# Kernel optimization log

Hardware: AMD Instinct MI355X
Metric: run time of the kernel (lower is better)

Reference implementation:

```python
import jax, jax.numpy as jnp
import numpy as np

N_HEADS, IN_F, COND_IN, OUT_F = 8, 16, 32, 32
B = 32768


def setup_inputs() -> dict:
    key = jax.random.key(0)
    k1, k2, k3, k4 = jax.random.split(key, 4)
    return {
        "input": jax.random.normal(k1, (N_HEADS, B, IN_F), dtype=jnp.float32),
        "cond": jax.random.normal(k2, (N_HEADS, B, COND_IN), dtype=jnp.float32),
        "cond_weight": jax.random.normal(k3, (N_HEADS, OUT_F * (IN_F + 1), COND_IN), dtype=jnp.float32) * 0.1,
        "cond_bias": jax.random.normal(k4, (N_HEADS, OUT_F * (IN_F + 1)), dtype=jnp.float32) * 0.1,
    }


def reference(input, cond, cond_weight, cond_bias):
    h, b, in_f = input.shape
    out_f = cond_weight.shape[1] // (in_f + 1)
    # hypernetwork: generate per-sample weights (h, b, out*(in+1))
    w = jnp.einsum('hbc,hkc->hbk', cond, cond_weight) + cond_bias[:, None, :]
    w = w.reshape(h, b, out_f, in_f + 1)  # (h, b, out, in+1)
    # append homogeneous 1 for bias column, then per-sample matvec
    x1 = jnp.concatenate([input, jnp.ones((h, b, 1), dtype=input.dtype)], axis=-1)
    return jnp.einsum('hboi,hbi->hbo', w, x1)
```

## Files before the change

kernel.cpp:

```cpp
#include <hip/hip_runtime.h>

#define NH    8
#define BROWS 32768
#define INF   16
#define CIN   32
#define OUTF  32
#define KTOT  544

typedef __attribute__((ext_vector_type(8))) short short8;
typedef __attribute__((ext_vector_type(4))) float floatx4;

__device__ __forceinline__ short f2bf(float f) {
    __bf16 h = (__bf16)f;
    return __builtin_bit_cast(short, h);
}

__global__ __launch_bounds__(256) void meta_multilinear(
    const float* __restrict__ input,
    const float* __restrict__ cond,
    const float* __restrict__ weight,
    const float* __restrict__ bias,
    float* __restrict__ out)
{
    const int tid   = threadIdx.x;
    const int lane  = tid & 63;
    const int wave  = tid >> 6;
    const int pair  = wave >> 1;
    const int otile = wave & 1;
    const int r     = lane & 15;
    const int quad  = lane >> 4;
    const int c0    = quad * 8;

    const int h = blockIdx.y;
    const int o = otile * 16 + r;

    const float* Wh = weight + (size_t)h * KTOT * CIN;
    const float* bh = bias   + (size_t)h * KTOT;

    short8 bfrag[17];
    #pragma unroll
    for (int i = 0; i < 17; ++i) {
        const float* src = Wh + (o * 17 + i) * CIN + c0;
        floatx4 w0 = *(const floatx4*)(src);
        floatx4 w1 = *(const floatx4*)(src + 4);
        short8 f;
        f[0]=f2bf(w0.x); f[1]=f2bf(w0.y); f[2]=f2bf(w0.z); f[3]=f2bf(w0.w);
        f[4]=f2bf(w1.x); f[5]=f2bf(w1.y); f[6]=f2bf(w1.z); f[7]=f2bf(w1.w);
        bfrag[i] = f;
    }

    short8 bbias;
    #pragma unroll
    for (int j = 0; j < 8; ++j) {
        const int i = c0 + j;
        short v = 0;
        if (i < 17) v = f2bf(bh[o * 17 + i]);
        bbias[j] = v;
    }

    const int pairId = blockIdx.x * 2 + pair;

    for (int it = 0; it < 8; ++it) {
        const int b0 = (pairId * 8 + it) * 16;

        const float* crow = cond + ((size_t)h * BROWS + b0 + r) * CIN + c0;
        floatx4 cA = *(const floatx4*)(crow);
        floatx4 cB = *(const floatx4*)(crow + 4);

        const float* xrow = input + ((size_t)h * BROWS + b0 + r) * INF;
        floatx4 x0 = *(const floatx4*)(xrow);
        floatx4 x1v = *(const floatx4*)(xrow + 4);
        floatx4 x2 = *(const floatx4*)(xrow + 8);
        floatx4 x3 = *(const floatx4*)(xrow + 12);
        const float xr[17] = {x0.x,x0.y,x0.z,x0.w, x1v.x,x1v.y,x1v.z,x1v.w,
                              x2.x,x2.y,x2.z,x2.w, x3.x,x3.y,x3.z,x3.w, 1.0f};

        floatx4 acc = {0.f, 0.f, 0.f, 0.f};

        {
            short8 af;
            if (quad == 0) {
                af[0]=f2bf(xr[0]); af[1]=f2bf(xr[1]); af[2]=f2bf(xr[2]); af[3]=f2bf(xr[3]);
                af[4]=f2bf(xr[4]); af[5]=f2bf(xr[5]); af[6]=f2bf(xr[6]); af[7]=f2bf(xr[7]);
            } else if (quad == 1) {
                af[0]=f2bf(xr[8]);  af[1]=f2bf(xr[9]);  af[2]=f2bf(xr[10]); af[3]=f2bf(xr[11]);
                af[4]=f2bf(xr[12]); af[5]=f2bf(xr[13]); af[6]=f2bf(xr[14]); af[7]=f2bf(xr[15]);
            } else if (quad == 2) {
                af[0]=f2bf(1.0f); af[1]=0; af[2]=0; af[3]=0;
                af[4]=0; af[5]=0; af[6]=0; af[7]=0;
            } else {
                af[0]=0; af[1]=0; af[2]=0; af[3]=0;
                af[4]=0; af[5]=0; af[6]=0; af[7]=0;
            }
            acc = __builtin_amdgcn_mfma_f32_16x16x32_bf16(af, bbias, acc, 0, 0, 0);
        }

        #pragma unroll
        for (int i = 0; i < 17; ++i) {
            const float s = xr[i];
            short8 af;
            af[0]=f2bf(cA.x*s); af[1]=f2bf(cA.y*s); af[2]=f2bf(cA.z*s); af[3]=f2bf(cA.w*s);
            af[4]=f2bf(cB.x*s); af[5]=f2bf(cB.y*s); af[6]=f2bf(cB.z*s); af[7]=f2bf(cB.w*s);
            acc = __builtin_amdgcn_mfma_f32_16x16x32_bf16(af, bfrag[i], acc, 0, 0, 0);
        }

        float* orow = out + ((size_t)h * BROWS + b0) * OUTF;
        #pragma unroll
        for (int j = 0; j < 4; ++j) {
            orow[(quad * 4 + j) * OUTF + o] = acc[j];
        }
    }
}

extern "C" void kernel_launch(void* const* d_in, const int* in_sizes, int n_in,
                              void* d_out, int out_size, void* d_ws, size_t ws_size,
                              hipStream_t stream) {
    const float* input  = (const float*)d_in[0];
    const float* cond   = (const float*)d_in[1];
    const float* weight = (const float*)d_in[2];
    const float* bias   = (const float*)d_in[3];
    float* out = (float*)d_out;

    dim3 grid(128, NH, 1);
    dim3 block(256, 1, 1);
    hipLaunchKernelGGL(meta_multilinear, grid, block, 0, stream,
                       input, cond, weight, bias, out);
}
```

Before: 133.7 us.

## Swap MFMA operands so output is transposed and scale per-column results by x

Restructures the per-sample computation so cond is converted to bf16 once per tile instead of being scaled by each input element before conversion. Each weight column's MFMA output is scaled by the input scalar in fp32 and accumulated into two alternating accumulators. The swapped operand order makes each lane own contiguous output columns, which allows vectorized 16-byte stores. The grid is doubled with half the iterations per wave, and launch bounds request higher occupancy. This adds fp32 vector FMAs after each MFMA in exchange for removing the per-element multiply and convert work.

```diff
diff --git a/kernel.cpp b/kernel.cpp
--- a/kernel.cpp
+++ b/kernel.cpp
@@ -15,7 +15,7 @@
     return __builtin_bit_cast(short, h);
 }
 
-__global__ __launch_bounds__(256) void meta_multilinear(
+__global__ __launch_bounds__(256, 3) void meta_multilinear(
     const float* __restrict__ input,
     const float* __restrict__ cond,
     const float* __restrict__ weight,
@@ -37,7 +37,7 @@
     const float* Wh = weight + (size_t)h * KTOT * CIN;
     const float* bh = bias   + (size_t)h * KTOT;
 
-    short8 bfrag[17];
+    short8 wfrag[17];
     #pragma unroll
     for (int i = 0; i < 17; ++i) {
         const float* src = Wh + (o * 17 + i) * CIN + c0;
@@ -46,69 +46,77 @@
         short8 f;
         f[0]=f2bf(w0.x); f[1]=f2bf(w0.y); f[2]=f2bf(w0.z); f[3]=f2bf(w0.w);
         f[4]=f2bf(w1.x); f[5]=f2bf(w1.y); f[6]=f2bf(w1.z); f[7]=f2bf(w1.w);
-        bfrag[i] = f;
+        wfrag[i] = f;
     }
 
-    short8 bbias;
+    short8 bA;
     #pragma unroll
     for (int j = 0; j < 8; ++j) {
         const int i = c0 + j;
         short v = 0;
         if (i < 17) v = f2bf(bh[o * 17 + i]);
-        bbias[j] = v;
+        bA[j] = v;
     }
 
     const int pairId = blockIdx.x * 2 + pair;
+    const int bbase  = pairId * 64;
 
-    for (int it = 0; it < 8; ++it) {
-        const int b0 = (pairId * 8 + it) * 16;
+    const float* condh = cond  + (size_t)h * BROWS * CIN;
+    const float* inh   = input + (size_t)h * BROWS * INF;
+    const floatx4 zero = {0.f, 0.f, 0.f, 0.f};
 
-        const float* crow = cond + ((size_t)h * BROWS + b0 + r) * CIN + c0;
+    #pragma unroll
+    for (int it = 0; it < 4; ++it) {
+        const int b0 = bbase + it * 16;
+
+        const float* crow = condh + (size_t)(b0 + r) * CIN + c0;
         floatx4 cA = *(const floatx4*)(crow);
         floatx4 cB = *(const floatx4*)(crow + 4);
 
-        const float* xrow = input + ((size_t)h * BROWS + b0 + r) * INF;
+        const float* xrow = inh + (size_t)(b0 + r) * INF;
         floatx4 x0 = *(const floatx4*)(xrow);
-        floatx4 x1v = *(const floatx4*)(xrow + 4);
+        floatx4 x1 = *(const floatx4*)(xrow + 4);
         floatx4 x2 = *(const floatx4*)(xrow + 8);
         floatx4 x3 = *(const floatx4*)(xrow + 12);
-        const float xr[17] = {x0.x,x0.y,x0.z,x0.w, x1v.x,x1v.y,x1v.z,x1v.w,
-                              x2.x,x2.y,x2.z,x2.w, x3.x,x3.y,x3.z,x3.w, 1.0f};
 
-        floatx4 acc = {0.f, 0.f, 0.f, 0.f};
+        short8 cf;
+        cf[0]=f2bf(cA.x); cf[1]=f2bf(cA.y); cf[2]=f2bf(cA.z); cf[3]=f2bf(cA.w);
+        cf[4]=f2bf(cB.x); cf[5]=f2bf(cB.y); cf[6]=f2bf(cB.z); cf[7]=f2bf(cB.w);
 
-        {
-            short8 af;
-            if (quad == 0) {
-                af[0]=f2bf(xr[0]); af[1]=f2bf(xr[1]); af[2]=f2bf(xr[2]); af[3]=f2bf(xr[3]);
-                af[4]=f2bf(xr[4]); af[5]=f2bf(xr[5]); af[6]=f2bf(xr[6]); af[7]=f2bf(xr[7]);
-            } else if (quad == 1) {
-                af[0]=f2bf(xr[8]);  af[1]=f2bf(xr[9]);  af[2]=f2bf(xr[10]); af[3]=f2bf(xr[11]);
-                af[4]=f2bf(xr[12]); af[5]=f2bf(xr[13]); af[6]=f2bf(xr[14]); af[7]=f2bf(xr[15]);
-            } else if (quad == 2) {
-                af[0]=f2bf(1.0f); af[1]=0; af[2]=0; af[3]=0;
-                af[4]=0; af[5]=0; af[6]=0; af[7]=0;
-            } else {
-                af[0]=0; af[1]=0; af[2]=0; af[3]=0;
-                af[4]=0; af[5]=0; af[6]=0; af[7]=0;
-            }
-            acc = __builtin_amdgcn_mfma_f32_16x16x32_bf16(af, bbias, acc, 0, 0, 0);
+        short8 xb;
+        if (quad == 0) {
+            xb[0]=f2bf(x0.x); xb[1]=f2bf(x0.y); xb[2]=f2bf(x0.z); xb[3]=f2bf(x0.w);
+            xb[4]=f2bf(x1.x); xb[5]=f2bf(x1.y); xb[6]=f2bf(x1.z); xb[7]=f2bf(x1.w);
+        } else if (quad == 1) {
+            xb[0]=f2bf(x2.x); xb[1]=f2bf(x2.y); xb[2]=f2bf(x2.z); xb[3]=f2bf(x2.w);
+            xb[4]=f2bf(x3.x); xb[5]=f2bf(x3.y); xb[6]=f2bf(x3.z); xb[7]=f2bf(x3.w);
+        } else if (quad == 2) {
+            xb[0]=f2bf(1.0f); xb[1]=0; xb[2]=0; xb[3]=0;
+            xb[4]=0; xb[5]=0; xb[6]=0; xb[7]=0;
+        } else {
+            xb[0]=0; xb[1]=0; xb[2]=0; xb[3]=0;
+            xb[4]=0; xb[5]=0; xb[6]=0; xb[7]=0;
         }
 
-        #pragma unroll
-        for (int i = 0; i < 17; ++i) {
-            const float s = xr[i];
-            short8 af;
-            af[0]=f2bf(cA.x*s); af[1]=f2bf(cA.y*s); af[2]=f2bf(cA.z*s); af[3]=f2bf(cA.w*s);
-            af[4]=f2bf(cB.x*s); af[5]=f2bf(cB.y*s); af[6]=f2bf(cB.z*s); af[7]=f2bf(cB.w*s);
-            acc = __builtin_amdgcn_mfma_f32_16x16x32_bf16(af, bfrag[i], acc, 0, 0, 0);
-        }
+        floatx4 f0 = __builtin_amdgcn_mfma_f32_16x16x32_bf16(bA, xb, zero, 0, 0, 0);
+        floatx4 f1 = zero;
 
-        float* orow = out + ((size_t)h * BROWS + b0) * OUTF;
-        #pragma unroll
-        for (int j = 0; j < 4; ++j) {
-            orow[(quad * 4 + j) * OUTF + o] = acc[j];
-        }
+        #define STEP(i, s) do { \
+            floatx4 d_ = __builtin_amdgcn_mfma_f32_16x16x32_bf16(wfrag[(i)], cf, zero, 0, 0, 0); \
+            if ((i) & 1) f1 += d_ * (s); else f0 += d_ * (s); \
+        } while (0)
+        STEP(0,  x0.x); STEP(1,  x0.y); STEP(2,  x0.z); STEP(3,  x0.w);
+        STEP(4,  x1.x); STEP(5,  x1.y); STEP(6,  x1.z); STEP(7,  x1.w);
+        STEP(8,  x2.x); STEP(9,  x2.y); STEP(10, x2.z); STEP(11, x2.w);
+        STEP(12, x3.x); STEP(13, x3.y); STEP(14, x3.z); STEP(15, x3.w);
+        STEP(16, 1.0f);
+        #undef STEP
+
+        const floatx4 facc = f0 + f1;
+
+        float* dst = out + ((size_t)h * BROWS + b0 + r) * OUTF
+                         + otile * 16 + quad * 4;
+        *(floatx4*)dst = facc;
     }
 }
 
@@ -121,7 +129,7 @@
     const float* bias   = (const float*)d_in[3];
     float* out = (float*)d_out;
 
-    dim3 grid(128, NH, 1);
+    dim3 grid(256, NH, 1);
     dim3 block(256, 1, 1);
     hipLaunchKernelGGL(meta_multilinear, grid, block, 0, stream,
                        input, cond, weight, bias, out);
```

Result: slower. 151.4 us (+13.3%).
